# Optimization experiments

Measured on AMD Instinct MI355X. Metric: run time of the kernel, lower is better.

The kernel has to match this reference:

```python
import jax, jax.numpy as jnp
import numpy as np

N_NODES = 50000
N_EDGES = 300000
ANNOT = 200
HID = 256
N_STEPS = 8
N_BRANCH = 2


def setup_inputs() -> dict:
    key = jax.random.key(0)
    ks = jax.random.split(key, 12)
    s = 0.05
    return {
        "x": jax.random.normal(ks[0], (N_NODES, ANNOT), dtype=jnp.float32),
        "edge_index": jax.random.randint(ks[1], (2, N_EDGES), 0, N_NODES, dtype=jnp.int32),
        "batch": jnp.zeros((N_NODES,), dtype=jnp.int32),
        "W_reduce": jax.random.normal(ks[2], (HID, ANNOT), dtype=jnp.float32) * s,
        "b_reduce": jnp.zeros((HID,), dtype=jnp.float32),
        "W_ggc": jax.random.normal(ks[3], (N_STEPS, HID, HID), dtype=jnp.float32) * s,
        "W_ih": jax.random.normal(ks[4], (3 * HID, HID), dtype=jnp.float32) * s,
        "W_hh": jax.random.normal(ks[5], (3 * HID, HID), dtype=jnp.float32) * s,
        "b_ih": jnp.zeros((3 * HID,), dtype=jnp.float32),
        "b_hh": jnp.zeros((3 * HID,), dtype=jnp.float32),
        "W_lin": jax.random.normal(ks[6], (N_BRANCH, HID), dtype=jnp.float32) * s,
        "b_lin": jnp.zeros((N_BRANCH,), dtype=jnp.float32),
    }


def _gru_cell(m, h, W_ih, W_hh, b_ih, b_hh):
    # PyTorch GRUCell: gates ordered r, z, n
    gi = m @ W_ih.T + b_ih  # [N, 3H]
    gh = h @ W_hh.T + b_hh
    i_r, i_z, i_n = jnp.split(gi, 3, axis=1)
    h_r, h_z, h_n = jnp.split(gh, 3, axis=1)
    r = jax.nn.sigmoid(i_r + h_r)
    z = jax.nn.sigmoid(i_z + h_z)
    n = jnp.tanh(i_n + r * h_n)
    return (1.0 - z) * n + z * h


def reference(x, edge_index, batch, W_reduce, b_reduce, W_ggc, W_ih, W_hh, b_ih, b_hh, W_lin, b_lin):
    del batch  # unused by forward math
    n = x.shape[0]
    src, dst = edge_index[0], edge_index[1]

    h = x @ W_reduce.T + b_reduce  # [N, H]

    def step(h, Wi):
        m = h @ Wi                                    # per-step linear [N, H]
        agg = jax.ops.segment_sum(m[src], dst, num_segments=n)  # scatter-add to targets
        h_new = _gru_cell(agg, h, W_ih, W_hh, b_ih, b_hh)
        return h_new, None

    h, _ = jax.lax.scan(step, h, W_ggc)

    out = jax.nn.relu(h) @ W_lin.T + b_lin  # [N, 2]
    return jax.nn.log_softmax(out, axis=1)
```

## Files before the change

kernel.cpp:

```cpp
#include <hip/hip_runtime.h>

typedef _Float16 f16;
typedef unsigned short u16;
typedef unsigned int u32;
typedef _Float16 f16x4 __attribute__((ext_vector_type(4)));
typedef _Float16 f16x8 __attribute__((ext_vector_type(8)));
typedef float    floatx4 __attribute__((ext_vector_type(4)));

#define N_NODES 50000
#define N_EDGES 300000
#define ANNOT   200
#define KXP     224
#define HID     256

__device__ __forceinline__ floatx4 mfma_16x16x32_f16(f16x8 a, f16x8 b, floatx4 c) {
#if defined(__HIP_DEVICE_COMPILE__)
    return __builtin_amdgcn_mfma_f32_16x16x32_f16(a, b, c, 0, 0, 0);
#else
    return c;
#endif
}
__device__ __forceinline__ void gload_lds16(const f16* g, f16* l) {
#if defined(__HIP_DEVICE_COMPILE__)
    __builtin_amdgcn_global_load_lds((const __attribute__((address_space(1))) void*)g,
                                     (__attribute__((address_space(3))) void*)l, 16, 0, 0);
#else
    (void)g; (void)l;
#endif
}

__device__ __forceinline__ float sigm(float x) { return 1.0f / (1.0f + __expf(-x)); }
__device__ __forceinline__ float tanh_fast(float x) { return 1.0f - 2.0f / (1.0f + __expf(2.0f * x)); }

__device__ __forceinline__ float bf_bits_to_f32(u16 u) {
    union { u32 i; float f; } v; v.i = ((u32)u) << 16; return v.f;
}
__device__ __forceinline__ u16 f32_to_bf_bits(float f) {
    union { float f; u32 i; } v; v.f = f;
    u32 b = v.i;
    b += 0x7FFFu + ((b >> 16) & 1u);
    return (u16)(b >> 16);
}
__device__ __forceinline__ float load_in(const void* p, long i, int flag) {
    if (flag) return ((const float*)p)[i];
    return bf_bits_to_f32(((const u16*)p)[i]);
}

__global__ void probe_dtype(const u32* __restrict__ xw, int* __restrict__ flag) {
    __shared__ int cnt;
    if (threadIdx.x == 0) cnt = 0;
    __syncthreads();
    int c = 0;
    for (int i = threadIdx.x; i < 256; i += 64) {
        u32 lo = xw[i] & 0xFFFFu;
        u32 e = (lo >> 7) & 0xFFu;
        if (e >= 105u && e <= 140u) c++;
    }
    atomicAdd(&cnt, c);
    __syncthreads();
    if (threadIdx.x == 0) flag[0] = (cnt > 128) ? 0 : 1;
}

__global__ void cvt_f16(const void* __restrict__ in, f16* __restrict__ out, int n,
                        const int* __restrict__ flagp) {
    const int flag = *flagp;
    const int i = blockIdx.x * 256 + threadIdx.x;
    if (i < n) out[i] = (f16)load_in(in, i, flag);
}

__global__ void build_wrT(const void* __restrict__ Wre, f16* __restrict__ WrT,
                          const int* __restrict__ flagp) {
    const int flag = *flagp;
    const int i = blockIdx.x * 256 + threadIdx.x;
    if (i >= 256 * KXP) return;
    const int n = i / KXP, k = i - n * KXP;
    WrT[i] = (k < ANNOT) ? (f16)load_in(Wre, (long)n * ANNOT + k, flag) : (f16)0.0f;
}

__global__ void build_bb8(const f16* __restrict__ Wc, const void* __restrict__ Whh,
                          f16* __restrict__ Bb, const int* __restrict__ flagp) {
    const int flag = *flagp;
    const int i = blockIdx.x * 256 + threadIdx.x;
    const int s = i >> 19;
    const int rem = i & 524287;
    const int row = rem >> 9;
    const int k = rem & 511;
    const int chblk = row >> 7;
    const int r = row & 127;
    const int g = r >> 5;
    const int c = r & 31;
    const int ch = chblk * 32 + c;
    f16 v = (f16)0.0f;
    if (g == 0) {
        v = (k < 256) ? Wc[(long)ch * 2048 + s * 256 + k]
                      : (f16)load_in(Whh, (long)ch * 256 + (k - 256), flag);
    } else if (g == 1) {
        v = (k < 256) ? Wc[(long)(256 + ch) * 2048 + s * 256 + k]
                      : (f16)load_in(Whh, (long)(256 + ch) * 256 + (k - 256), flag);
    } else if (g == 2) {
        if (k < 256) v = Wc[(long)(512 + ch) * 2048 + s * 256 + k];
    } else {
        if (k >= 256) v = (f16)load_in(Whh, (long)(512 + ch) * 256 + (k - 256), flag);
    }
    Bb[i] = v;
}

__global__ void build_small(const void* b_ih, const void* b_hh, const void* b_red,
                            const void* W_lin, const void* b_lin,
                            float* __restrict__ sp, const int* __restrict__ flagp) {
    const int flag = *flagp;
    const int i = blockIdx.x * 256 + threadIdx.x;
    if (i < 512) {
        sp[i] = load_in(b_ih, i, flag) + load_in(b_hh, i, flag);
    } else if (i < 768) {
        sp[i] = load_in(b_ih, 512 + (i - 512), flag);
    } else if (i < 1024) {
        sp[i] = load_in(b_hh, 512 + (i - 768), flag);
    } else if (i < 1280) {
        sp[i] = load_in(b_red, i - 1024, flag);
    } else if (i < 1792) {
        sp[i] = load_in(W_lin, i - 1280, flag);
    } else if (i < 1794) {
        sp[i] = load_in(b_lin, i - 1792, flag);
    }
}

__global__ void build_xcvt(const void* __restrict__ x, f16* __restrict__ xc,
                           const int* __restrict__ flagp) {
    const int flag = *flagp;
    const long i = (long)blockIdx.x * 256 + threadIdx.x;
    if (i >= (long)N_NODES * KXP) return;
    const long r = i / KXP;
    const int  k = (int)(i - r * KXP);
    xc[i] = (k < ANNOT) ? (f16)load_in(x, r * ANNOT + k, flag) : (f16)0.0f;
}

__global__ void zero_i32(int* __restrict__ p, int n) {
    const int i = blockIdx.x * 256 + threadIdx.x;
    if (i < n) p[i] = 0;
}
__global__ void hist_kernel(const int* __restrict__ dst, int* __restrict__ deg, int n) {
    const int e = blockIdx.x * 256 + threadIdx.x;
    if (e < n) atomicAdd(&deg[dst[e]], 1);
}
__global__ void block_sum(const int* __restrict__ deg, int* __restrict__ partial, int n) {
    __shared__ int s[256];
    const int i = blockIdx.x * 256 + threadIdx.x;
    s[threadIdx.x] = (i < n) ? deg[i] : 0;
    __syncthreads();
    for (int off = 128; off > 0; off >>= 1) {
        if (threadIdx.x < off) s[threadIdx.x] += s[threadIdx.x + off];
        __syncthreads();
    }
    if (threadIdx.x == 0) partial[blockIdx.x] = s[0];
}
__global__ void scan_partials(int* __restrict__ partial, int nb, int* __restrict__ total_out) {
    __shared__ int s[256];
    const int t = threadIdx.x;
    s[t] = (t < nb) ? partial[t] : 0;
    __syncthreads();
    for (int off = 1; off < 256; off <<= 1) {
        int v = (t >= off) ? s[t - off] : 0;
        __syncthreads();
        s[t] += v;
        __syncthreads();
    }
    if (t < nb) partial[t] = (t == 0) ? 0 : s[t - 1];
    if (t == 0) *total_out = s[255];
}
__global__ void scan_block(const int* __restrict__ deg, const int* __restrict__ partial,
                           int* __restrict__ row_off, int* __restrict__ cursor, int n) {
    __shared__ int s[256];
    const int t = threadIdx.x;
    const int i = blockIdx.x * 256 + t;
    const int v = (i < n) ? deg[i] : 0;
    s[t] = v;
    __syncthreads();
    for (int off = 1; off < 256; off <<= 1) {
        int u = (t >= off) ? s[t - off] : 0;
        __syncthreads();
        s[t] += u;
        __syncthreads();
    }
    if (i < n) {
        const int v0 = partial[blockIdx.x] + s[t] - v;
        row_off[i] = v0;
        cursor[i]  = v0;
    }
}
__global__ void fill_kernel(const int* __restrict__ src, const int* __restrict__ dst,
                            int* __restrict__ cursor, int* __restrict__ csr, int n) {
    const int e = blockIdx.x * 256 + threadIdx.x;
    if (e < n) {
        const int p = atomicAdd(&cursor[dst[e]], 1);
        csr[p] = src[e];
    }
}

__global__ __launch_bounds__(256) void mgemm(
    const f16* __restrict__ A, int lda,
    const f16* __restrict__ Bt, int ldb,
    f16* __restrict__ C, int ldc,
    const float* __restrict__ bias,
    int M, int N, int K)
{
    __shared__ __attribute__((aligned(16))) f16 As[128 * 32];
    __shared__ __attribute__((aligned(16))) f16 Bs[128 * 32];
    const int tid  = threadIdx.x;
    const int lane = tid & 63;
    const int wave = tid >> 6;
    const int bm = blockIdx.x * 128;
    const int bn = blockIdx.y * 128;
    const int wm = (wave >> 1) * 64;
    const int wn = (wave & 1) * 64;
    const int quad = lane >> 4;
    const int l16  = lane & 15;

    floatx4 acc[4][4];
#pragma unroll
    for (int i = 0; i < 4; ++i)
#pragma unroll
        for (int j = 0; j < 4; ++j) acc[i][j] = (floatx4)(0.0f);

    for (int k0 = 0; k0 < K; k0 += 32) {
        __syncthreads();
#pragma unroll
        for (int it = 0; it < 2; ++it) {
            const int ci  = it * 256 + tid;
            const int row = ci >> 2;
            const int cg  = ci & 3;
            int ga = bm + row; if (ga > M - 1) ga = M - 1;
            gload_lds16(A + (long)ga * lda + k0 + cg * 8, As + ci * 8);
            gload_lds16(Bt + (long)(bn + row) * ldb + k0 + cg * 8, Bs + ci * 8);
        }
        __syncthreads();

        f16x8 af[4], bfv[4];
#pragma unroll
        for (int i = 0; i < 4; ++i) {
            af[i]  = *(const f16x8*)(As + (wm + i * 16 + l16) * 32 + quad * 8);
            bfv[i] = *(const f16x8*)(Bs + (wn + i * 16 + l16) * 32 + quad * 8);
        }
#pragma unroll
        for (int i = 0; i < 4; ++i)
#pragma unroll
            for (int j = 0; j < 4; ++j)
                acc[i][j] = mfma_16x16x32_f16(af[i], bfv[j], acc[i][j]);
    }

#pragma unroll
    for (int i = 0; i < 4; ++i) {
        const int r0 = bm + wm + i * 16 + quad * 4;
#pragma unroll
        for (int j = 0; j < 4; ++j) {
            const int col = bn + wn + j * 16 + l16;
            const float bv = bias ? bias[col] : 0.0f;
#pragma unroll
            for (int v = 0; v < 4; ++v) {
                const int r = r0 + v;
                if (r < M) C[(long)r * ldc + col] = (f16)(acc[i][j][v] + bv);
            }
        }
    }
}

__global__ __launch_bounds__(256) void gemm_gates(
    const f16* __restrict__ agh, const f16* __restrict__ Bb,
    f16* __restrict__ agh_nxt,
    const float* __restrict__ brz, const float* __restrict__ bin,
    const float* __restrict__ bhn, int M)
{
    const int lin = blockIdx.x;
    const int within = lin & 63;
    const int rb = (lin >> 6) * 8 + (within & 7);
    const int cb = within >> 3;
    if (rb * 128 >= M) return;

    __shared__ __attribute__((aligned(16))) f16 As[128 * 32];
    __shared__ __attribute__((aligned(16))) f16 Bs[128 * 32];
    const int tid  = threadIdx.x;
    const int lane = tid & 63;
    const int wave = tid >> 6;
    const int bm = rb * 128;
    const int wm  = (wave >> 1) * 64;
    const int chh = (wave & 1) * 16;
    const int quad = lane >> 4;
    const int l16  = lane & 15;
    const int k_cap = 256 + cb * 32;

    floatx4 acc[4][4];
#pragma unroll
    for (int i = 0; i < 4; ++i)
#pragma unroll
        for (int j = 0; j < 4; ++j) acc[i][j] = (floatx4)(0.0f);
    f16 h_frag[4][4] = {};

    for (int k0 = 0; k0 < 512; k0 += 32) {
        __syncthreads();
#pragma unroll
        for (int it = 0; it < 2; ++it) {
            const int ci  = it * 256 + tid;
            const int row = ci >> 2;
            const int cg  = ci & 3;
            int ga = bm + row; if (ga > M - 1) ga = M - 1;
            gload_lds16(agh + (long)ga * 512 + k0 + cg * 8, As + ci * 8);
            gload_lds16(Bb + (long)(cb * 128 + row) * 512 + k0 + cg * 8, Bs + ci * 8);
        }
        __syncthreads();

        if (k0 == k_cap) {
#pragma unroll
            for (int i = 0; i < 4; ++i)
#pragma unroll
                for (int v = 0; v < 4; ++v)
                    h_frag[i][v] = As[(wm + i * 16 + quad * 4 + v) * 32 + chh + l16];
        }

        f16x8 af[4], bfv[4];
#pragma unroll
        for (int i = 0; i < 4; ++i) {
            af[i]  = *(const f16x8*)(As + (wm + i * 16 + l16) * 32 + quad * 8);
            bfv[i] = *(const f16x8*)(Bs + (i * 32 + chh + l16) * 32 + quad * 8);
        }
#pragma unroll
        for (int i = 0; i < 4; ++i)
#pragma unroll
            for (int j = 0; j < 4; ++j)
                acc[i][j] = mfma_16x16x32_f16(af[i], bfv[j], acc[i][j]);
    }

    const int ch = cb * 32 + chh + l16;
    const float b_r  = brz[ch];
    const float b_z  = brz[256 + ch];
    const float b_in = bin[ch];
    const float b_hn = bhn[ch];
#pragma unroll
    for (int i = 0; i < 4; ++i) {
        const int r0 = bm + wm + i * 16 + quad * 4;
#pragma unroll
        for (int v = 0; v < 4; ++v) {
            const int r = r0 + v;
            if (r < M) {
                const float rg = sigm(acc[i][0][v] + b_r);
                const float zg = sigm(acc[i][1][v] + b_z);
                const float nn = tanh_fast(acc[i][2][v] + b_in + rg * (acc[i][3][v] + b_hn));
                const float ho = (float)h_frag[i][v];
                agh_nxt[(long)r * 512 + 256 + ch] = (f16)((1.0f - zg) * nn + zg * ho);
            }
        }
    }
}

__global__ __launch_bounds__(256) void aggregate(
    f16* __restrict__ agh, const int* __restrict__ row_off, const int* __restrict__ csr)
{
    const int node = blockIdx.x * 8 + (threadIdx.x >> 5);
    const int lane = threadIdx.x & 31;
    if (node >= N_NODES) return;
    const int e0 = row_off[node], e1 = row_off[node + 1];
    float a[8] = {0.0f, 0.0f, 0.0f, 0.0f, 0.0f, 0.0f, 0.0f, 0.0f};
    for (int e = e0; e < e1; ++e) {
        const int s = csr[e];
        const f16x8 v = *(const f16x8*)(agh + (long)s * 512 + 256 + lane * 8);
#pragma unroll
        for (int u = 0; u < 8; ++u) a[u] += (float)v[u];
    }
    f16x8 o;
#pragma unroll
    for (int u = 0; u < 8; ++u) o[u] = (f16)a[u];
    *(f16x8*)(agh + (long)node * 512 + lane * 8) = o;
}

__global__ __launch_bounds__(256) void final_kernel(
    const f16* __restrict__ h, const float* __restrict__ wlin,
    const float* __restrict__ blin, void* __restrict__ out,
    const int* __restrict__ flagp)
{
    const int flag = *flagp;
    const int node = blockIdx.x * 4 + (threadIdx.x >> 6);
    const int lane = threadIdx.x & 63;
    if (node >= N_NODES) return;
    const f16* hp = h + (long)node * 512;
    float a0 = 0.0f, a1 = 0.0f;
#pragma unroll
    for (int u = 0; u < 4; ++u) {
        const int c = lane * 4 + u;
        float hv = (float)hp[c];
        hv = hv > 0.0f ? hv : 0.0f;
        a0 += hv * wlin[c];
        a1 += hv * wlin[256 + c];
    }
#pragma unroll
    for (int off = 32; off > 0; off >>= 1) {
        a0 += __shfl_down(a0, off);
        a1 += __shfl_down(a1, off);
    }
    if (lane == 0) {
        a0 += blin[0];
        a1 += blin[1];
        const float mx  = fmaxf(a0, a1);
        const float lse = mx + logf(expf(a0 - mx) + expf(a1 - mx));
        const float o0 = a0 - lse, o1 = a1 - lse;
        if (flag) {
            ((float*)out)[(long)node * 2]     = o0;
            ((float*)out)[(long)node * 2 + 1] = o1;
        } else {
            ((u16*)out)[(long)node * 2]     = f32_to_bf_bits(o0);
            ((u16*)out)[(long)node * 2 + 1] = f32_to_bf_bits(o1);
        }
    }
}

extern "C" void kernel_launch(void* const* d_in, const int* in_sizes, int n_in,
                              void* d_out, int out_size, void* d_ws, size_t ws_size,
                              hipStream_t stream)
{
    (void)in_sizes; (void)n_in; (void)out_size; (void)ws_size;
    const void* x        = d_in[0];
    const int*  ei       = (const int*)d_in[1];
    const void* W_reduce = d_in[3];
    const void* b_reduce = d_in[4];
    const void* W_ggc    = d_in[5];
    const void* W_ih     = d_in[6];
    const void* W_hh     = d_in[7];
    const void* b_ih     = d_in[8];
    const void* b_hh     = d_in[9];
    const void* W_lin    = d_in[10];
    const void* b_lin    = d_in[11];
    const int* src = ei;
    const int* dst = ei + N_EDGES;

    char* w = (char*)d_ws;
    auto carve = [&](size_t bytes) -> char* {
        char* p = w;
        w += (bytes + 255) & ~(size_t)255;
        return p;
    };
    f16* agh_a = (f16*)carve((size_t)N_NODES * 512 * 2);
    f16* agh_b = (f16*)carve((size_t)N_NODES * 512 * 2);
    f16* x_cvt = agh_b;
    f16*   WrT   = (f16*)carve((size_t)256 * KXP * 2);
    f16*   Wih16 = (f16*)carve((size_t)768 * 256 * 2);
    f16*   Wg16  = (f16*)carve((size_t)2048 * 256 * 2);
    f16*   Wc    = (f16*)carve((size_t)768 * 2048 * 2);
    f16*   Bb8   = (f16*)carve((size_t)8 * 1024 * 512 * 2);
    float* sp    = (float*)carve(2048 * 4);
    int*   flag  = (int*)carve(256);
    int* deg     = (int*)carve((size_t)N_NODES * 4);
    int* row_off = (int*)carve((size_t)(N_NODES + 1) * 4);
    int* cursor  = (int*)carve((size_t)N_NODES * 4);
    int* csr     = (int*)carve((size_t)N_EDGES * 4);
    int* partial = (int*)carve(256 * 4);

    float* brz  = sp;
    float* bin  = sp + 512;
    float* bhn  = sp + 768;
    float* br0  = sp + 1024;
    float* wlin = sp + 1280;
    float* blin = sp + 1792;

    probe_dtype<<<1, 64, 0, stream>>>((const u32*)x, flag);

    cvt_f16<<<(768 * 256 + 255) / 256, 256, 0, stream>>>(W_ih, Wih16, 768 * 256, flag);
    cvt_f16<<<(2048 * 256 + 255) / 256, 256, 0, stream>>>(W_ggc, Wg16, 2048 * 256, flag);
    build_wrT<<<(256 * KXP + 255) / 256, 256, 0, stream>>>(W_reduce, WrT, flag);
    build_small<<<8, 256, 0, stream>>>(b_ih, b_hh, b_reduce, W_lin, b_lin, sp, flag);
    build_xcvt<<<(int)(((long)N_NODES * KXP + 255) / 256), 256, 0, stream>>>(x, x_cvt, flag);

    zero_i32<<<196, 256, 0, stream>>>(deg, N_NODES);
    hist_kernel<<<(N_EDGES + 255) / 256, 256, 0, stream>>>(dst, deg, N_EDGES);
    block_sum<<<196, 256, 0, stream>>>(deg, partial, N_NODES);
    scan_partials<<<1, 256, 0, stream>>>(partial, 196, row_off + N_NODES);
    scan_block<<<196, 256, 0, stream>>>(deg, partial, row_off, cursor, N_NODES);
    fill_kernel<<<(N_EDGES + 255) / 256, 256, 0, stream>>>(src, dst, cursor, csr, N_EDGES);

    mgemm<<<dim3(6, 16), 256, 0, stream>>>(Wih16, 256, Wg16, 256, Wc, 2048,
                                           (const float*)nullptr, 768, 2048, 256);
    build_bb8<<<(8 * 1024 * 512) / 256, 256, 0, stream>>>(Wc, W_hh, Bb8, flag);

    mgemm<<<dim3(391, 2), 256, 0, stream>>>(x_cvt, KXP, WrT, KXP, agh_a + 256, 512, br0,
                                            N_NODES, 256, KXP);

    for (int s = 0; s < 8; ++s) {
        f16* cur = (s & 1) ? agh_b : agh_a;
        f16* nxt = (s & 1) ? agh_a : agh_b;
        aggregate<<<6250, 256, 0, stream>>>(cur, row_off, csr);
        gemm_gates<<<49 * 64, 256, 0, stream>>>(cur, Bb8 + (size_t)s * 524288, nxt,
                                                brz, bin, bhn, N_NODES);
    }

    final_kernel<<<12500, 256, 0, stream>>>(agh_a + 256, wlin, blin, d_out, flag);
}
```

Baseline: 1.265 ms.

## Skip zero gate blocks in GRU gate GEMM, widen K tile, swizzle LDS

```diff
diff --git a/kernel.cpp b/kernel.cpp
--- a/kernel.cpp
+++ b/kernel.cpp
@@ -264,6 +264,41 @@
     }
 }
 
+
+#define GATES_STAGE(K0)                                                             \
+    {                                                                               \
+        __syncthreads();                                                            \
+        _Pragma("unroll")                                                           \
+        for (int it_ = 0; it_ < 4; ++it_) {                                         \
+            const int ci_  = it_ * 256 + tid;                                       \
+            const int row_ = ci_ >> 3;                                              \
+            const int lc_  = (ci_ & 7) ^ (row_ & 7);                                \
+            int ga_ = bm + row_; if (ga_ > M - 1) ga_ = M - 1;                      \
+            gload_lds16(agh + (long)ga_ * 512 + (K0) + lc_ * 8, As + ci_ * 8);      \
+            gload_lds16(Bb + (long)(cb * 128 + row_) * 512 + (K0) + lc_ * 8,        \
+                        Bs + ci_ * 8);                                              \
+        }                                                                           \
+        __syncthreads();                                                            \
+    }
+
+#define GATES_STEP(KC, JJ)                                                          \
+    {                                                                               \
+        const int sl_ = (((KC) >> 3) + quad) ^ xr;                                  \
+        f16x8 af_[4];                                                               \
+        _Pragma("unroll")                                                           \
+        for (int i_ = 0; i_ < 4; ++i_)                                              \
+            af_[i_] = *(const f16x8*)(As + (wm + i_ * 16 + l16) * 64 + sl_ * 8);    \
+        const f16x8 b0_ = *(const f16x8*)(Bs + (chh + l16) * 64 + sl_ * 8);         \
+        const f16x8 b1_ = *(const f16x8*)(Bs + (32 + chh + l16) * 64 + sl_ * 8);    \
+        const f16x8 b2_ = *(const f16x8*)(Bs + ((JJ) * 32 + chh + l16) * 64 + sl_ * 8); \
+        _Pragma("unroll")                                                           \
+        for (int i_ = 0; i_ < 4; ++i_) {                                            \
+            acc[i_][0]    = mfma_16x16x32_f16(af_[i_], b0_, acc[i_][0]);            \
+            acc[i_][1]    = mfma_16x16x32_f16(af_[i_], b1_, acc[i_][1]);            \
+            acc[i_][(JJ)] = mfma_16x16x32_f16(af_[i_], b2_, acc[i_][(JJ)]);         \
+        }                                                                           \
+    }
+
 __global__ __launch_bounds__(256) void gemm_gates(
     const f16* __restrict__ agh, const f16* __restrict__ Bb,
     f16* __restrict__ agh_nxt,
@@ -276,8 +311,8 @@
     const int cb = within >> 3;
     if (rb * 128 >= M) return;
 
-    __shared__ __attribute__((aligned(16))) f16 As[128 * 32];
-    __shared__ __attribute__((aligned(16))) f16 Bs[128 * 32];
+    __shared__ __attribute__((aligned(16))) f16 As[128 * 64];
+    __shared__ __attribute__((aligned(16))) f16 Bs[128 * 64];
     const int tid  = threadIdx.x;
     const int lane = tid & 63;
     const int wave = tid >> 6;
@@ -286,7 +321,9 @@
     const int chh = (wave & 1) * 16;
     const int quad = lane >> 4;
     const int l16  = lane & 15;
-    const int k_cap = 256 + cb * 32;
+    const int xr   = l16 & 7;
+    const int kcap0 = 256 + ((cb * 32) & ~63);
+    const int koff  = (cb & 1) * 32;
 
     floatx4 acc[4][4];
 #pragma unroll
@@ -295,38 +332,26 @@
         for (int j = 0; j < 4; ++j) acc[i][j] = (floatx4)(0.0f);
     f16 h_frag[4][4] = {};
 
-    for (int k0 = 0; k0 < 512; k0 += 32) {
-        __syncthreads();
-#pragma unroll
-        for (int it = 0; it < 2; ++it) {
-            const int ci  = it * 256 + tid;
-            const int row = ci >> 2;
-            const int cg  = ci & 3;
-            int ga = bm + row; if (ga > M - 1) ga = M - 1;
-            gload_lds16(agh + (long)ga * 512 + k0 + cg * 8, As + ci * 8);
-            gload_lds16(Bb + (long)(cb * 128 + row) * 512 + k0 + cg * 8, Bs + ci * 8);
+    for (int k0 = 0; k0 < 256; k0 += 64) {
+        GATES_STAGE(k0)
+        GATES_STEP(0, 2)
+        GATES_STEP(32, 2)
+    }
+    for (int k0 = 256; k0 < 512; k0 += 64) {
+        GATES_STAGE(k0)
+        if (k0 == kcap0) {
+#pragma unroll
+            for (int i = 0; i < 4; ++i)
+#pragma unroll
+                for (int v = 0; v < 4; ++v) {
+                    const int r = wm + i * 16 + quad * 4 + v;
+                    const int kcol = koff + chh + l16;
+                    const int slot = (kcol >> 3) ^ (r & 7);
+                    h_frag[i][v] = As[r * 64 + slot * 8 + (kcol & 7)];
+                }
         }
-        __syncthreads();
-
-        if (k0 == k_cap) {
-#pragma unroll
-            for (int i = 0; i < 4; ++i)
-#pragma unroll
-                for (int v = 0; v < 4; ++v)
-                    h_frag[i][v] = As[(wm + i * 16 + quad * 4 + v) * 32 + chh + l16];
-        }
-
-        f16x8 af[4], bfv[4];
-#pragma unroll
-        for (int i = 0; i < 4; ++i) {
-            af[i]  = *(const f16x8*)(As + (wm + i * 16 + l16) * 32 + quad * 8);
-            bfv[i] = *(const f16x8*)(Bs + (i * 32 + chh + l16) * 32 + quad * 8);
-        }
-#pragma unroll
-        for (int i = 0; i < 4; ++i)
-#pragma unroll
-            for (int j = 0; j < 4; ++j)
-                acc[i][j] = mfma_16x16x32_f16(af[i], bfv[j], acc[i][j]);
+        GATES_STEP(0, 3)
+        GATES_STEP(32, 3)
     }
 
     const int ch = cb * 32 + chh + l16;
```

After: 1.157 ms. -8.6%, faster.

## Skip zero blocks in gates GEMM via direct global fragment loads; unroll aggregation

Applied to the files above, without the earlier changes.

```diff
diff --git a/kernel.cpp b/kernel.cpp
--- a/kernel.cpp
+++ b/kernel.cpp
@@ -276,8 +276,6 @@
     const int cb = within >> 3;
     if (rb * 128 >= M) return;
 
-    __shared__ __attribute__((aligned(16))) f16 As[128 * 32];
-    __shared__ __attribute__((aligned(16))) f16 Bs[128 * 32];
     const int tid  = threadIdx.x;
     const int lane = tid & 63;
     const int wave = tid >> 6;
@@ -286,47 +284,52 @@
     const int chh = (wave & 1) * 16;
     const int quad = lane >> 4;
     const int l16  = lane & 15;
-    const int k_cap = 256 + cb * 32;
+
+    const f16* ap[4];
+#pragma unroll
+    for (int i = 0; i < 4; ++i) {
+        int r = bm + wm + i * 16 + l16;
+        if (r > M - 1) r = M - 1;
+        ap[i] = agh + (long)r * 512 + quad * 8;
+    }
+    const f16* b0p = Bb + (long)(cb * 128 +      chh + l16) * 512 + quad * 8;
+    const f16* b1p = Bb + (long)(cb * 128 + 32 + chh + l16) * 512 + quad * 8;
+    const f16* b2p = Bb + (long)(cb * 128 + 64 + chh + l16) * 512 + quad * 8;
+    const f16* b3p = Bb + (long)(cb * 128 + 96 + chh + l16) * 512 + quad * 8;
 
     floatx4 acc[4][4];
 #pragma unroll
     for (int i = 0; i < 4; ++i)
 #pragma unroll
         for (int j = 0; j < 4; ++j) acc[i][j] = (floatx4)(0.0f);
-    f16 h_frag[4][4] = {};
-
-    for (int k0 = 0; k0 < 512; k0 += 32) {
-        __syncthreads();
-#pragma unroll
-        for (int it = 0; it < 2; ++it) {
-            const int ci  = it * 256 + tid;
-            const int row = ci >> 2;
-            const int cg  = ci & 3;
-            int ga = bm + row; if (ga > M - 1) ga = M - 1;
-            gload_lds16(agh + (long)ga * 512 + k0 + cg * 8, As + ci * 8);
-            gload_lds16(Bb + (long)(cb * 128 + row) * 512 + k0 + cg * 8, Bs + ci * 8);
-        }
-        __syncthreads();
-
-        if (k0 == k_cap) {
-#pragma unroll
-            for (int i = 0; i < 4; ++i)
-#pragma unroll
-                for (int v = 0; v < 4; ++v)
-                    h_frag[i][v] = As[(wm + i * 16 + quad * 4 + v) * 32 + chh + l16];
-        }
-
-        f16x8 af[4], bfv[4];
+
+#pragma unroll
+    for (int kt = 0; kt < 8; ++kt) {
+        const int k = kt * 32;
+        const f16x8 b0 = *(const f16x8*)(b0p + k);
+        const f16x8 b1 = *(const f16x8*)(b1p + k);
+        const f16x8 b2 = *(const f16x8*)(b2p + k);
 #pragma unroll
         for (int i = 0; i < 4; ++i) {
-            af[i]  = *(const f16x8*)(As + (wm + i * 16 + l16) * 32 + quad * 8);
-            bfv[i] = *(const f16x8*)(Bs + (i * 32 + chh + l16) * 32 + quad * 8);
-        }
-#pragma unroll
-        for (int i = 0; i < 4; ++i)
-#pragma unroll
-            for (int j = 0; j < 4; ++j)
-                acc[i][j] = mfma_16x16x32_f16(af[i], bfv[j], acc[i][j]);
+            const f16x8 a = *(const f16x8*)(ap[i] + k);
+            acc[i][0] = mfma_16x16x32_f16(a, b0, acc[i][0]);
+            acc[i][1] = mfma_16x16x32_f16(a, b1, acc[i][1]);
+            acc[i][2] = mfma_16x16x32_f16(a, b2, acc[i][2]);
+        }
+    }
+#pragma unroll
+    for (int kt = 8; kt < 16; ++kt) {
+        const int k = kt * 32;
+        const f16x8 b0 = *(const f16x8*)(b0p + k);
+        const f16x8 b1 = *(const f16x8*)(b1p + k);
+        const f16x8 b3 = *(const f16x8*)(b3p + k);
+#pragma unroll
+        for (int i = 0; i < 4; ++i) {
+            const f16x8 a = *(const f16x8*)(ap[i] + k);
+            acc[i][0] = mfma_16x16x32_f16(a, b0, acc[i][0]);
+            acc[i][1] = mfma_16x16x32_f16(a, b1, acc[i][1]);
+            acc[i][3] = mfma_16x16x32_f16(a, b3, acc[i][3]);
+        }
     }
 
     const int ch = cb * 32 + chh + l16;
@@ -344,7 +347,7 @@
                 const float rg = sigm(acc[i][0][v] + b_r);
                 const float zg = sigm(acc[i][1][v] + b_z);
                 const float nn = tanh_fast(acc[i][2][v] + b_in + rg * (acc[i][3][v] + b_hn));
-                const float ho = (float)h_frag[i][v];
+                const float ho = (float)agh[(long)r * 512 + 256 + ch];
                 agh_nxt[(long)r * 512 + 256 + ch] = (f16)((1.0f - zg) * nn + zg * ho);
             }
         }
@@ -359,15 +362,25 @@
     if (node >= N_NODES) return;
     const int e0 = row_off[node], e1 = row_off[node + 1];
     float a[8] = {0.0f, 0.0f, 0.0f, 0.0f, 0.0f, 0.0f, 0.0f, 0.0f};
-    for (int e = e0; e < e1; ++e) {
-        const int s = csr[e];
-        const f16x8 v = *(const f16x8*)(agh + (long)s * 512 + 256 + lane * 8);
-#pragma unroll
-        for (int u = 0; u < 8; ++u) a[u] += (float)v[u];
+    float b[8] = {0.0f, 0.0f, 0.0f, 0.0f, 0.0f, 0.0f, 0.0f, 0.0f};
+    int e = e0;
+    for (; e + 2 <= e1; e += 2) {
+        const int s0 = csr[e];
+        const int s1 = csr[e + 1];
+        const f16x8 v0 = *(const f16x8*)(agh + (long)s0 * 512 + 256 + lane * 8);
+        const f16x8 v1 = *(const f16x8*)(agh + (long)s1 * 512 + 256 + lane * 8);
+#pragma unroll
+        for (int u = 0; u < 8; ++u) { a[u] += (float)v0[u]; b[u] += (float)v1[u]; }
+    }
+    if (e < e1) {
+        const int s0 = csr[e];
+        const f16x8 v0 = *(const f16x8*)(agh + (long)s0 * 512 + 256 + lane * 8);
+#pragma unroll
+        for (int u = 0; u < 8; ++u) a[u] += (float)v0[u];
     }
     f16x8 o;
 #pragma unroll
-    for (int u = 0; u < 8; ++u) o[u] = (f16)a[u];
+    for (int u = 0; u < 8; ++u) o[u] = (f16)(a[u] + b[u]);
     *(f16x8*)(agh + (long)node * 512 + lane * 8) = o;
 }
 
```

Measured after the change: 1.818 ms. +43.7%, slower.
